# Kernel tuning notes

Hardware: AMD Instinct MI355X
Metric: run time of the kernel (lower is better)

Reference implementation:

```python
import jax, jax.numpy as jnp
import numpy as np

B, T, RES, C = 4, 8, 32, 128
TSP, SPLIT = 4, 4
NH_BRANCH = 4  # num_heads // 2 per branch
HID = 4 * C


def layer_norm(x, w, b, eps=1e-5):
    mu = x.mean(-1, keepdims=True)
    var = ((x - mu) ** 2).mean(-1, keepdims=True)
    return (x - mu) * jax.lax.rsqrt(var + eps) * w + b


def dwconv3d(x, w, b):
    # x: (Bw, C, Tsp, Hsp, Wsp); w: (C, 1, 3, 3, 3) depthwise
    y = jax.lax.conv_general_dilated(
        x, w, (1, 1, 1), 'SAME',
        dimension_numbers=('NCDHW', 'OIDHW', 'NCDHW'),
        feature_group_count=x.shape[1])
    return y + b[None, :, None, None, None]


def lepe_attention(q, k, v, conv_w, conv_b, Tsp, Hsp, Wsp, nh, Tt, H, W):
    Bq, L, Cc = q.shape
    hd = Cc // nh
    win = Tsp * Hsp * Wsp
    scale = float(hd) ** -0.5

    def to_win(z):
        z = z.reshape(Bq, Tt // Tsp, Tsp, H // Hsp, Hsp, W // Wsp, Wsp, Cc)
        z = z.transpose(0, 1, 3, 5, 2, 4, 6, 7).reshape(-1, win, nh, hd)
        return z.transpose(0, 2, 1, 3)

    qw = to_win(q) * scale
    kw = to_win(k)
    # v windows as (Bw, C, Tsp, Hsp, Wsp) for the depthwise-conv LePE
    vw5 = v.reshape(Bq, Tt // Tsp, Tsp, H // Hsp, Hsp, W // Wsp, Wsp, Cc)
    vw5 = vw5.transpose(0, 1, 3, 5, 7, 2, 4, 6).reshape(-1, Cc, Tsp, Hsp, Wsp)
    lepe = dwconv3d(vw5, conv_w, conv_b)

    def heads(z5):
        return z5.reshape(-1, nh, hd, win).transpose(0, 1, 3, 2)

    vh, lepeh = heads(vw5), heads(lepe)
    attn = jax.nn.softmax(jnp.einsum('bnqd,bnkd->bnqk', qw, kw), axis=-1)
    out = jnp.einsum('bnqk,bnkd->bnqd', attn, vh) + lepeh
    # windows -> video token order (T, H, W)
    out = out.transpose(0, 2, 1, 3).reshape(
        Bq, Tt // Tsp, H // Hsp, W // Wsp, Tsp, Hsp, Wsp, Cc)
    out = out.transpose(0, 1, 4, 2, 5, 3, 6, 7).reshape(Bq, L, Cc)
    return out


def setup_inputs() -> dict:
    key = jax.random.key(0)
    ks = jax.random.split(key, 16)
    L = T * RES * RES
    h = C // 2
    p = lambda k, s: jax.random.normal(k, s, dtype=jnp.float32) * 0.02
    return {
        'x': jax.random.normal(ks[0], (B, L, C), dtype=jnp.float32),
        'norm1_w': jnp.ones((C,), jnp.float32),
        'norm1_b': jnp.zeros((C,), jnp.float32),
        'qkv_w': p(ks[1], (3 * C, C)),
        'conv_w0': p(ks[2], (h, 1, 3, 3, 3)),
        'conv_b0': jnp.zeros((h,), jnp.float32),
        'conv_w1': p(ks[3], (h, 1, 3, 3, 3)),
        'conv_b1': jnp.zeros((h,), jnp.float32),
        'proj_w': p(ks[4], (C, C)),
        'proj_b': jnp.zeros((C,), jnp.float32),
        'norm2_w': jnp.ones((C,), jnp.float32),
        'norm2_b': jnp.zeros((C,), jnp.float32),
        'fc1_w': p(ks[5], (HID, C)),
        'fc1_b': jnp.zeros((HID,), jnp.float32),
        'fc2_w': p(ks[6], (C, HID)),
        'fc2_b': jnp.zeros((C,), jnp.float32),
    }


def reference(x, norm1_w, norm1_b, qkv_w, conv_w0, conv_b0, conv_w1, conv_b1,
              proj_w, proj_b, norm2_w, norm2_b, fc1_w, fc1_b, fc2_w, fc2_b):
    img = layer_norm(x, norm1_w, norm1_b)
    qkv = img @ qkv_w.T  # (B, L, 3C), split order q, k, v
    q, k, v = jnp.split(qkv, 3, axis=-1)
    h = C // 2
    # branch 0 (idx=0): H_sp = reso, W_sp = split_size
    x1 = lepe_attention(q[..., :h], k[..., :h], v[..., :h], conv_w0, conv_b0,
                        TSP, RES, SPLIT, NH_BRANCH, T, RES, RES)
    # branch 1 (idx=1): H_sp = split_size, W_sp = reso
    x2 = lepe_attention(q[..., h:], k[..., h:], v[..., h:], conv_w1, conv_b1,
                        TSP, SPLIT, RES, NH_BRANCH, T, RES, RES)
    att = jnp.concatenate([x1, x2], axis=2) @ proj_w.T + proj_b
    x = x + att
    y = layer_norm(x, norm2_w, norm2_b)
    y = jax.nn.gelu(y @ fc1_w.T + fc1_b, approximate=False) @ fc2_w.T + fc2_b
    return x + y
```

## Files before the change

kernel.cpp:

```cpp
#include <hip/hip_runtime.h>
#include <math.h>

namespace {
constexpr int C_ = 128;
constexpr int BL = 32768;

typedef __attribute__((ext_vector_type(4))) float f32x4;
typedef __attribute__((ext_vector_type(4))) _Float16 f16x4;
typedef __attribute__((ext_vector_type(8))) _Float16 f16x8;
typedef __attribute__((ext_vector_type(2))) __fp16 hf2;

#if __has_builtin(__builtin_amdgcn_exp2f)
#define EXP2F(x) __builtin_amdgcn_exp2f(x)
#else
#define EXP2F(x) exp2f(x)
#endif
}

__global__ __launch_bounds__(256) void k_cvt(
    const float* __restrict__ qkvw, const float* __restrict__ pw,
    const float* __restrict__ f1w,  const float* __restrict__ f2w,
    const float* __restrict__ cw0,  const float* __restrict__ cw1,
    _Float16* __restrict__ wqh, _Float16* __restrict__ pwh,
    _Float16* __restrict__ w1h, _Float16* __restrict__ w2h,
    float* __restrict__ lepw)
{
  int i = blockIdx.x * 256 + threadIdx.x;
  if (i < 49152) {
    float v = qkvw[i];
    if (i < 16384) v *= 0.360673762f;
    wqh[i] = (_Float16)v;
  }
  else if (i < 65536)  pwh[i - 49152] = (_Float16)pw[i - 49152];
  else if (i < 131072) w1h[i - 65536] = (_Float16)f1w[i - 65536];
  else if (i < 196608) w2h[i - 131072] = (_Float16)f2w[i - 131072];
  else if (i < 200064) {
    int j = i - 196608;
    int br = j / 1728, r = j % 1728, widx = r >> 6, ch = r & 63;
    lepw[j] = (br ? cw1 : cw0)[ch * 27 + widx];
  }
}

__global__ __launch_bounds__(256) void k_ln_qkv(
    const float* __restrict__ x,
    const float* __restrict__ nw,
    const float* __restrict__ nb,
    const _Float16* __restrict__ wqh,
    _Float16* __restrict__ qh, _Float16* __restrict__ kh, _Float16* __restrict__ vh)
{
  __shared__ _Float16 xs[64][136];
  __shared__ _Float16 qt[64][136];
  __shared__ _Float16 wbuf[128][136];
  const int tid = threadIdx.x;
  const int row0 = blockIdx.x << 6;
  const int bb = row0 >> 13, t = (row0 >> 10) & 7, h0 = (row0 >> 5) & 31;
  const int tb = t >> 2, t_in = t & 3;

  {
    const int r = tid >> 2, j = tid & 3;
    const float* xp = x + (size_t)(row0 + r) * C_ + j * 32;
    float v[32];
#pragma unroll
    for (int i = 0; i < 8; ++i) {
      float4 u = ((const float4*)xp)[i];
      v[i*4+0] = u.x; v[i*4+1] = u.y; v[i*4+2] = u.z; v[i*4+3] = u.w;
    }
    float s1 = 0.f, s2 = 0.f;
#pragma unroll
    for (int i = 0; i < 32; ++i) { s1 += v[i]; s2 += v[i] * v[i]; }
    s1 += __shfl_down(s1, 2, 4); s1 += __shfl_down(s1, 1, 4);
    s2 += __shfl_down(s2, 2, 4); s2 += __shfl_down(s2, 1, 4);
    float mu = __shfl(s1, 0, 4) * (1.f / 128.f);
    float ms = __shfl(s2, 0, 4) * (1.f / 128.f);
    float rstd = rsqrtf(ms - mu * mu + 1e-5f);
#pragma unroll
    for (int i = 0; i < 32; ++i) {
      int c = j * 32 + i;
      xs[r][c] = (_Float16)((v[i] - mu) * rstd * nw[c] + nb[c]);
    }
  }
  __syncthreads();

  const int lane = tid & 63, wave = tid >> 6;
  const int m0 = wave << 4, mi = lane & 15, quad = lane >> 4;

  f16x8 afr[4];
#pragma unroll
  for (int kt = 0; kt < 4; ++kt)
    afr[kt] = *(const f16x8*)&xs[m0 + mi][kt * 32 + quad * 8];

  for (int g = 0; g < 3; ++g) {
#pragma unroll
    for (int it = 0; it < 8; ++it) {
      int id = it * 256 + tid;
      int r = id >> 4, c8 = id & 15;
      *(uint4*)&wbuf[r][c8 * 8] = *(const uint4*)(wqh + (size_t)(g * 128 + r) * 128 + c8 * 8);
    }
    __syncthreads();

    f32x4 acc[8];
#pragma unroll
    for (int nt = 0; nt < 8; ++nt) acc[nt] = (f32x4){0.f, 0.f, 0.f, 0.f};
#pragma unroll
    for (int nt = 0; nt < 8; ++nt) {
#pragma unroll
      for (int kt = 0; kt < 4; ++kt) {
        f16x8 bfr = *(const f16x8*)&wbuf[nt * 16 + mi][kt * 32 + quad * 8];
        acc[nt] = __builtin_amdgcn_mfma_f32_16x16x32_f16(afr[kt], bfr, acc[nt], 0, 0, 0);
      }
    }
#pragma unroll
    for (int nt = 0; nt < 8; ++nt) {
      int n = nt * 16 + mi;
#pragma unroll
      for (int rr = 0; rr < 4; ++rr)
        qt[m0 + quad * 4 + rr][n] = (_Float16)acc[nt][rr];
    }
    __syncthreads();

    _Float16* G = (g == 0) ? qh : (g == 1) ? kh : vh;
#pragma unroll
    for (int it = 0; it < 4; ++it) {
      int u = it * 256 + tid;
      if (u < 512) {
        int half = u & 1, p = (u >> 1) & 7, head = (u >> 4) & 3, sb = u >> 6;
        int token = (p >> 2) * 32 + sb * 4 + (p & 3);
        uint4 d = *(const uint4*)&qt[token][head * 16 + half * 8];
        int win = bb * 16 + tb * 8 + sb;
        int pos = t_in * 128 + h0 * 4 + p;
        *(uint4*)(G + ((size_t)(head * 64 + win) * 512 + pos) * 16 + half * 8) = d;
      } else {
        int u2 = u - 512;
        int half = u2 & 1, pin = (u2 >> 1) & 63, head = u2 >> 7;
        uint4 d = *(const uint4*)&qt[pin][64 + head * 16 + half * 8];
        int win = bb * 16 + tb * 8 + (h0 >> 2);
        int pos = t_in * 128 + (h0 & 3) * 32 + pin;
        *(uint4*)(G + ((size_t)((4 + head) * 64 + win) * 512 + pos) * 16 + half * 8) = d;
      }
    }
    __syncthreads();
  }
}

__global__ __launch_bounds__(512) void k_attn(
    const _Float16* __restrict__ qh,
    const _Float16* __restrict__ kh,
    const _Float16* __restrict__ vh,
    const float* __restrict__ lepw,
    const float* __restrict__ cb0,
    const float* __restrict__ cb1,
    _Float16* __restrict__ attnh)
{
  __shared__ _Float16 Ks[512][20];
  __shared__ _Float16 Vs[512][20];

  const int tid = threadIdx.x;
  const int bid = blockIdx.x;
  const int br = bid >> 8, wi = (bid >> 2) & 63, head = bid & 3;
  const int b = wi >> 4, tb = (wi >> 3) & 1, sb = wi & 7;
  const int coff = br * 64 + head * 16;
  const int Hsp = br ? 4 : 32, Wsp = br ? 32 : 4;
  const float* cb = br ? cb1 : cb0;
  const size_t base = ((size_t)(br * 4 + head) * 64 + wi) * 512 * 16;

  auto token_of = [&](int p) -> int {
    int t_in = p >> 7;
    int rem = p & 127;
    int h, w;
    if (br == 0) { h = rem >> 2;            w = sb * 4 + (rem & 3); }
    else         { h = sb * 4 + (rem >> 5); w = rem & 31; }
    return ((b * 8 + tb * 4 + t_in) << 10) + (h << 5) + w;
  };

  {
    const int r = tid;
    const _Float16* kp = kh + base + r * 16;
    const _Float16* vp = vh + base + r * 16;
    f16x8 k0 = *(const f16x8*)kp;
    f16x8 k1 = *(const f16x8*)(kp + 8);
    f16x8 v0 = *(const f16x8*)vp;
    f16x8 v1 = *(const f16x8*)(vp + 8);
    *(f16x4*)&Ks[r][0]  = (f16x4){k0[0], k0[1], k0[2], k0[3]};
    *(f16x4*)&Ks[r][4]  = (f16x4){k0[4], k0[5], k0[6], k0[7]};
    *(f16x4*)&Ks[r][8]  = (f16x4){k1[0], k1[1], k1[2], k1[3]};
    *(f16x4*)&Ks[r][12] = (f16x4){k1[4], k1[5], k1[6], k1[7]};
    *(f16x4*)&Vs[r][0]  = (f16x4){v0[0], v0[1], v0[2], v0[3]};
    *(f16x4*)&Vs[r][4]  = (f16x4){v0[4], v0[5], v0[6], v0[7]};
    *(f16x4*)&Vs[r][8]  = (f16x4){v1[0], v1[1], v1[2], v1[3]};
    *(f16x4*)&Vs[r][12] = (f16x4){v1[4], v1[5], v1[6], v1[7]};
  }

  const int lane = tid & 63, wave = tid >> 6;
  const int mi = lane & 15, quad = lane >> 4;

  int qtok[4];
  f16x4 qfr[4];
#pragma unroll
  for (int qi = 0; qi < 4; ++qi) {
    int q = (wave * 4 + qi) * 16 + mi;
    qtok[qi] = token_of(q);
    qfr[qi] = *(const f16x4*)(qh + base + q * 16 + quad * 4);
  }
  __syncthreads();

  f32x4 acc[4];
  float l[4];
#pragma unroll
  for (int qi = 0; qi < 4; ++qi) { acc[qi] = (f32x4){0.f,0.f,0.f,0.f}; l[qi] = 0.f; }

  const hf2 one2 = {(__fp16)1.f, (__fp16)1.f};

  for (int kt = 0; kt < 32; ++kt) {
    const int kb = kt << 4;
    f16x4 kfr = *(const f16x4*)&Ks[kb + mi][quad * 4];
    f16x4 vfr;
    vfr[0] = Vs[kb + quad * 4 + 0][mi];
    vfr[1] = Vs[kb + quad * 4 + 1][mi];
    vfr[2] = Vs[kb + quad * 4 + 2][mi];
    vfr[3] = Vs[kb + quad * 4 + 3][mi];
#pragma unroll
    for (int qi = 0; qi < 4; ++qi) {
      f32x4 s = __builtin_amdgcn_mfma_f32_16x16x16f16(kfr, qfr[qi], (f32x4){0.f,0.f,0.f,0.f}, 0, 0, 0);
      float p0 = EXP2F(s[0]);
      float p1 = EXP2F(s[1]);
      float p2 = EXP2F(s[2]);
      float p3 = EXP2F(s[3]);
      hf2 plo = __builtin_amdgcn_cvt_pkrtz(p0, p1);
      hf2 phi = __builtin_amdgcn_cvt_pkrtz(p2, p3);
#if __has_builtin(__builtin_amdgcn_fdot2)
      l[qi] = __builtin_amdgcn_fdot2(plo, one2, l[qi], false);
      l[qi] = __builtin_amdgcn_fdot2(phi, one2, l[qi], false);
#else
      l[qi] += (p0 + p1) + (p2 + p3);
#endif
      union { struct { hf2 lo, hi; } h; f16x4 v; } u;
      u.h.lo = plo; u.h.hi = phi;
      acc[qi] = __builtin_amdgcn_mfma_f32_16x16x16f16(vfr, u.v, acc[qi], 0, 0, 0);
    }
  }

#pragma unroll
  for (int qi = 0; qi < 4; ++qi) {
    float lq = l[qi];
    lq += __shfl_xor(lq, 16, 64);
    lq += __shfl_xor(lq, 32, 64);
    float inv = 1.f / lq;

    const int q = (wave * 4 + qi) * 16 + mi;
    int t_in = q >> 7, rem = q & 127;
    int h_in, w_in;
    if (br == 0) { h_in = rem >> 2; w_in = rem & 3; }
    else         { h_in = rem >> 5; w_in = rem & 31; }
    float4 lep = *(const float4*)(cb + head * 16 + quad * 4);
    for (int dz = 0; dz < 3; ++dz) {
      int tz = t_in + dz - 1; if ((unsigned)tz >= 4u) continue;
      for (int dy = 0; dy < 3; ++dy) {
        int ty = h_in + dy - 1; if ((unsigned)ty >= (unsigned)Hsp) continue;
        for (int dx = 0; dx < 3; ++dx) {
          int tx = w_in + dx - 1; if ((unsigned)tx >= (unsigned)Wsp) continue;
          int np = (tz * Hsp + ty) * Wsp + tx;
          int widx = (dz * 3 + dy) * 3 + dx;
          float4 w4 = *(const float4*)(lepw + ((br * 27 + widx) << 6) + head * 16 + quad * 4);
          f16x4 vv = *(const f16x4*)&Vs[np][quad * 4];
          lep.x += w4.x * (float)vv[0];
          lep.y += w4.y * (float)vv[1];
          lep.z += w4.z * (float)vv[2];
          lep.w += w4.w * (float)vv[3];
        }
      }
    }
    f16x4 ov;
    ov[0] = (_Float16)(acc[qi][0] * inv + lep.x);
    ov[1] = (_Float16)(acc[qi][1] * inv + lep.y);
    ov[2] = (_Float16)(acc[qi][2] * inv + lep.z);
    ov[3] = (_Float16)(acc[qi][3] * inv + lep.w);
    *(f16x4*)(attnh + (size_t)qtok[qi] * 128 + coff + quad * 4) = ov;
  }
}

__global__ __launch_bounds__(256) void k_proj(
    const _Float16* __restrict__ attnh,
    const _Float16* __restrict__ pwh,
    const float* __restrict__ pb,
    const float* __restrict__ x,
    _Float16* __restrict__ xrh)
{
  __shared__ _Float16 as_[64][136];
  __shared__ _Float16 wbuf[128][136];
  const int tid = threadIdx.x;
  const int row0 = blockIdx.x << 6;

#pragma unroll
  for (int it = 0; it < 4; ++it) {
    int id = it * 256 + tid;
    int r = id >> 4, c8 = id & 15;
    *(uint4*)&as_[r][c8 * 8] = *(const uint4*)(attnh + (size_t)(row0 + r) * 128 + c8 * 8);
  }
#pragma unroll
  for (int it = 0; it < 8; ++it) {
    int id = it * 256 + tid;
    int r = id >> 4, c8 = id & 15;
    *(uint4*)&wbuf[r][c8 * 8] = *(const uint4*)(pwh + (size_t)r * 128 + c8 * 8);
  }
  __syncthreads();

  const int lane = tid & 63, wave = tid >> 6;
  const int m0 = wave << 4, mi = lane & 15, quad = lane >> 4;

  f16x8 afr[4];
#pragma unroll
  for (int kt = 0; kt < 4; ++kt)
    afr[kt] = *(const f16x8*)&as_[m0 + mi][kt * 32 + quad * 8];

  f32x4 acc[8];
#pragma unroll
  for (int nt = 0; nt < 8; ++nt) acc[nt] = (f32x4){0.f, 0.f, 0.f, 0.f};
#pragma unroll
  for (int nt = 0; nt < 8; ++nt) {
#pragma unroll
    for (int kt = 0; kt < 4; ++kt) {
      f16x8 bfr = *(const f16x8*)&wbuf[nt * 16 + mi][kt * 32 + quad * 8];
      acc[nt] = __builtin_amdgcn_mfma_f32_16x16x32_f16(afr[kt], bfr, acc[nt], 0, 0, 0);
    }
  }
  __syncthreads();
#pragma unroll
  for (int nt = 0; nt < 8; ++nt) {
    int n = nt * 16 + mi;
    float bb = pb[n];
#pragma unroll
    for (int rr = 0; rr < 4; ++rr)
      as_[m0 + quad * 4 + rr][n] = (_Float16)(acc[nt][rr] + bb);
  }
  __syncthreads();

#pragma unroll
  for (int it = 0; it < 4; ++it) {
    int id = it * 256 + tid;
    int r = id >> 4, c8 = id & 15;
    f16x8 v = *(const f16x8*)&as_[r][c8 * 8];
    const float* xp = x + (size_t)(row0 + r) * 128 + c8 * 8;
    float4 xa = *(const float4*)xp;
    float4 xb = *(const float4*)(xp + 4);
    f16x8 o;
    o[0] = (_Float16)((float)v[0] + xa.x); o[1] = (_Float16)((float)v[1] + xa.y);
    o[2] = (_Float16)((float)v[2] + xa.z); o[3] = (_Float16)((float)v[3] + xa.w);
    o[4] = (_Float16)((float)v[4] + xb.x); o[5] = (_Float16)((float)v[5] + xb.y);
    o[6] = (_Float16)((float)v[6] + xb.z); o[7] = (_Float16)((float)v[7] + xb.w);
    *(f16x8*)(xrh + (size_t)(row0 + r) * 128 + c8 * 8) = o;
  }
}

__global__ __launch_bounds__(256) void k_mlp(
    const _Float16* __restrict__ xrh,
    const float* __restrict__ nw,
    const float* __restrict__ nb,
    const _Float16* __restrict__ w1h,
    const float* __restrict__ f1b,
    const _Float16* __restrict__ w2h,
    const float* __restrict__ f2b,
    float* __restrict__ out)
{
  __shared__ _Float16 xs[64][136];
  __shared__ _Float16 wbuf[128][136];
  const int tid = threadIdx.x;
  const int row0 = blockIdx.x << 6;

  {
    const int r = tid >> 2, j = tid & 3;
    const _Float16* xp = xrh + (size_t)(row0 + r) * C_ + j * 32;
    float v[32];
#pragma unroll
    for (int i = 0; i < 4; ++i) {
      f16x8 u = ((const f16x8*)xp)[i];
#pragma unroll
      for (int k = 0; k < 8; ++k) v[i * 8 + k] = (float)u[k];
    }
    float s1 = 0.f, s2 = 0.f;
#pragma unroll
    for (int i = 0; i < 32; ++i) { s1 += v[i]; s2 += v[i] * v[i]; }
    s1 += __shfl_down(s1, 2, 4); s1 += __shfl_down(s1, 1, 4);
    s2 += __shfl_down(s2, 2, 4); s2 += __shfl_down(s2, 1, 4);
    float mu = __shfl(s1, 0, 4) * (1.f / 128.f);
    float ms = __shfl(s2, 0, 4) * (1.f / 128.f);
    float rstd = rsqrtf(ms - mu * mu + 1e-5f);
#pragma unroll
    for (int i = 0; i < 32; ++i) {
      int c = j * 32 + i;
      xs[r][c] = (_Float16)((v[i] - mu) * rstd * nw[c] + nb[c]);
    }
  }
  __syncthreads();

  const int lane = tid & 63, wave = tid >> 6;
  const int tok0 = wave << 4, mi = lane & 15, quad = lane >> 4;

  f16x8 bx[4];
#pragma unroll
  for (int kt = 0; kt < 4; ++kt)
    bx[kt] = *(const f16x8*)&xs[tok0 + mi][kt * 32 + quad * 8];

  f32x4 oacc[8];
#pragma unroll
  for (int o = 0; o < 8; ++o) oacc[o] = (f32x4){0.f, 0.f, 0.f, 0.f};

  for (int ng = 0; ng < 4; ++ng) {
#pragma unroll
    for (int it = 0; it < 8; ++it) {
      int id = it * 256 + tid;
      int r = id >> 4, c8 = id & 15;
      *(uint4*)&wbuf[r][c8 * 8] = *(const uint4*)(w1h + (size_t)(ng * 128 + r) * 128 + c8 * 8);
    }
    __syncthreads();

    f32x4 hacc[8];
#pragma unroll
    for (int t = 0; t < 8; ++t) hacc[t] = (f32x4){0.f, 0.f, 0.f, 0.f};
#pragma unroll
    for (int t = 0; t < 8; ++t) {
#pragma unroll
      for (int kt = 0; kt < 4; ++kt) {
        f16x8 wfr = *(const f16x8*)&wbuf[t * 16 + mi][kt * 32 + quad * 8];
        hacc[t] = __builtin_amdgcn_mfma_f32_16x16x32_f16(wfr, bx[kt], hacc[t], 0, 0, 0);
      }
    }
    f16x4 ph[8];
#pragma unroll
    for (int t = 0; t < 8; ++t) {
      float4 bj = *(const float4*)(f1b + ng * 128 + t * 16 + quad * 4);
      float h0v = hacc[t][0] + bj.x;
      float h1v = hacc[t][1] + bj.y;
      float h2v = hacc[t][2] + bj.z;
      float h3v = hacc[t][3] + bj.w;
      ph[t][0] = (_Float16)(0.5f * h0v * (1.f + erff(h0v * 0.70710678118654752f)));
      ph[t][1] = (_Float16)(0.5f * h1v * (1.f + erff(h1v * 0.70710678118654752f)));
      ph[t][2] = (_Float16)(0.5f * h2v * (1.f + erff(h2v * 0.70710678118654752f)));
      ph[t][3] = (_Float16)(0.5f * h3v * (1.f + erff(h3v * 0.70710678118654752f)));
    }
    __syncthreads();

#pragma unroll
    for (int it = 0; it < 8; ++it) {
      int id = it * 256 + tid;
      int r = id >> 4, c8 = id & 15;
      *(uint4*)&wbuf[r][c8 * 8] = *(const uint4*)(w2h + (size_t)r * 512 + ng * 128 + c8 * 8);
    }
    __syncthreads();

#pragma unroll
    for (int o = 0; o < 8; ++o) {
#pragma unroll
      for (int t = 0; t < 8; ++t) {
        f16x4 wfr = *(const f16x4*)&wbuf[o * 16 + mi][t * 16 + quad * 4];
        oacc[o] = __builtin_amdgcn_mfma_f32_16x16x16f16(wfr, ph[t], oacc[o], 0, 0, 0);
      }
    }
    __syncthreads();
  }

#pragma unroll
  for (int o = 0; o < 8; ++o) {
    int row = row0 + tok0 + mi;
    int cb4 = o * 16 + quad * 4;
    float4 bo = *(const float4*)(f2b + cb4);
    f16x4 res = *(const f16x4*)(xrh + (size_t)row * C_ + cb4);
    float4 ov;
    ov.x = oacc[o][0] + bo.x + (float)res[0];
    ov.y = oacc[o][1] + bo.y + (float)res[1];
    ov.z = oacc[o][2] + bo.z + (float)res[2];
    ov.w = oacc[o][3] + bo.w + (float)res[3];
    *(float4*)(out + (size_t)row * C_ + cb4) = ov;
  }
}

extern "C" void kernel_launch(void* const* d_in, const int* in_sizes, int n_in,
                              void* d_out, int out_size, void* d_ws, size_t ws_size,
                              hipStream_t stream)
{
  const float* x    = (const float*)d_in[0];
  const float* n1w  = (const float*)d_in[1];
  const float* n1b  = (const float*)d_in[2];
  const float* qkvw = (const float*)d_in[3];
  const float* cw0  = (const float*)d_in[4];
  const float* cb0  = (const float*)d_in[5];
  const float* cw1  = (const float*)d_in[6];
  const float* cb1  = (const float*)d_in[7];
  const float* pw   = (const float*)d_in[8];
  const float* pb   = (const float*)d_in[9];
  const float* n2w  = (const float*)d_in[10];
  const float* n2b  = (const float*)d_in[11];
  const float* f1w  = (const float*)d_in[12];
  const float* f1b  = (const float*)d_in[13];
  const float* f2w  = (const float*)d_in[14];
  const float* f2b  = (const float*)d_in[15];

  char* ws = (char*)d_ws;
  _Float16* qh    = (_Float16*)ws;
  _Float16* kh    = (_Float16*)(ws +  8388608);
  _Float16* vh    = (_Float16*)(ws + 16777216);
  _Float16* attnh = (_Float16*)(ws + 25165824);
  _Float16* xrh   = (_Float16*)(ws + 33554432);
  _Float16* wqh   = (_Float16*)(ws + 41943040);
  _Float16* pwh   = (_Float16*)(ws + 42041344);
  _Float16* w1h   = (_Float16*)(ws + 42074112);
  _Float16* w2h   = (_Float16*)(ws + 42205184);
  float*    lepw  = (float*)   (ws + 42336256);

  k_cvt   <<<782,     256, 0, stream>>>(qkvw, pw, f1w, f2w, cw0, cw1,
                                        wqh, pwh, w1h, w2h, lepw);
  k_ln_qkv<<<BL / 64, 256, 0, stream>>>(x, n1w, n1b, wqh, qh, kh, vh);
  k_attn  <<<512,     512, 0, stream>>>(qh, kh, vh, lepw, cb0, cb1, attnh);
  k_proj  <<<BL / 64, 256, 0, stream>>>(attnh, pwh, pb, x, xrh);
  k_mlp   <<<BL / 64, 256, 0, stream>>>(xrh, n2w, n2b, w1h, f1b, w2h, f2b,
                                        (float*)d_out);
}
```

Baseline: 197.1 us.

## Halve row tile to 32 tokens and split N across waves in GEMM kernels

The LN+QKV, projection and MLP kernels now process 32 rows per block instead of 64, with the four waves arranged as 2 M-tiles by 2 N-halves. This doubles the grid size to 1024 blocks so more blocks can be resident across the CUs, and it halves per-wave accumulator registers. The cost is that every weight tile in LDS is loaded twice as often per token, which adds global and LDS traffic. The head scatter in the QKV kernel is remapped for the smaller tile.

```diff
diff --git a/kernel.cpp b/kernel.cpp
--- a/kernel.cpp
+++ b/kernel.cpp
@@ -48,41 +48,42 @@
     const _Float16* __restrict__ wqh,
     _Float16* __restrict__ qh, _Float16* __restrict__ kh, _Float16* __restrict__ vh)
 {
-  __shared__ _Float16 xs[64][136];
-  __shared__ _Float16 qt[64][136];
+  __shared__ _Float16 xs[32][136];
+  __shared__ _Float16 qt[32][136];
   __shared__ _Float16 wbuf[128][136];
   const int tid = threadIdx.x;
-  const int row0 = blockIdx.x << 6;
+  const int row0 = blockIdx.x << 5;
   const int bb = row0 >> 13, t = (row0 >> 10) & 7, h0 = (row0 >> 5) & 31;
   const int tb = t >> 2, t_in = t & 3;
 
   {
-    const int r = tid >> 2, j = tid & 3;
-    const float* xp = x + (size_t)(row0 + r) * C_ + j * 32;
-    float v[32];
-#pragma unroll
-    for (int i = 0; i < 8; ++i) {
+    const int r = tid >> 3, j = tid & 7;
+    const float* xp = x + (size_t)(row0 + r) * C_ + j * 16;
+    float v[16];
+#pragma unroll
+    for (int i = 0; i < 4; ++i) {
       float4 u = ((const float4*)xp)[i];
       v[i*4+0] = u.x; v[i*4+1] = u.y; v[i*4+2] = u.z; v[i*4+3] = u.w;
     }
     float s1 = 0.f, s2 = 0.f;
 #pragma unroll
-    for (int i = 0; i < 32; ++i) { s1 += v[i]; s2 += v[i] * v[i]; }
-    s1 += __shfl_down(s1, 2, 4); s1 += __shfl_down(s1, 1, 4);
-    s2 += __shfl_down(s2, 2, 4); s2 += __shfl_down(s2, 1, 4);
-    float mu = __shfl(s1, 0, 4) * (1.f / 128.f);
-    float ms = __shfl(s2, 0, 4) * (1.f / 128.f);
+    for (int i = 0; i < 16; ++i) { s1 += v[i]; s2 += v[i] * v[i]; }
+    s1 += __shfl_down(s1, 4, 8); s1 += __shfl_down(s1, 2, 8); s1 += __shfl_down(s1, 1, 8);
+    s2 += __shfl_down(s2, 4, 8); s2 += __shfl_down(s2, 2, 8); s2 += __shfl_down(s2, 1, 8);
+    float mu = __shfl(s1, 0, 8) * (1.f / 128.f);
+    float ms = __shfl(s2, 0, 8) * (1.f / 128.f);
     float rstd = rsqrtf(ms - mu * mu + 1e-5f);
 #pragma unroll
-    for (int i = 0; i < 32; ++i) {
-      int c = j * 32 + i;
+    for (int i = 0; i < 16; ++i) {
+      int c = j * 16 + i;
       xs[r][c] = (_Float16)((v[i] - mu) * rstd * nw[c] + nb[c]);
     }
   }
   __syncthreads();
 
   const int lane = tid & 63, wave = tid >> 6;
-  const int m0 = wave << 4, mi = lane & 15, quad = lane >> 4;
+  const int mt = wave & 1, nh = wave >> 1;
+  const int m0 = mt << 4, mi = lane & 15, quad = lane >> 4;
 
   f16x8 afr[4];
 #pragma unroll
@@ -98,20 +99,21 @@
     }
     __syncthreads();
 
-    f32x4 acc[8];
-#pragma unroll
-    for (int nt = 0; nt < 8; ++nt) acc[nt] = (f32x4){0.f, 0.f, 0.f, 0.f};
-#pragma unroll
-    for (int nt = 0; nt < 8; ++nt) {
+    f32x4 acc[4];
+#pragma unroll
+    for (int nt = 0; nt < 4; ++nt) acc[nt] = (f32x4){0.f, 0.f, 0.f, 0.f};
+#pragma unroll
+    for (int nt = 0; nt < 4; ++nt) {
+      int wrow = (nh * 4 + nt) * 16 + mi;
 #pragma unroll
       for (int kt = 0; kt < 4; ++kt) {
-        f16x8 bfr = *(const f16x8*)&wbuf[nt * 16 + mi][kt * 32 + quad * 8];
+        f16x8 bfr = *(const f16x8*)&wbuf[wrow][kt * 32 + quad * 8];
         acc[nt] = __builtin_amdgcn_mfma_f32_16x16x32_f16(afr[kt], bfr, acc[nt], 0, 0, 0);
       }
     }
 #pragma unroll
-    for (int nt = 0; nt < 8; ++nt) {
-      int n = nt * 16 + mi;
+    for (int nt = 0; nt < 4; ++nt) {
+      int n = (nh * 4 + nt) * 16 + mi;
 #pragma unroll
       for (int rr = 0; rr < 4; ++rr)
         qt[m0 + quad * 4 + rr][n] = (_Float16)acc[nt][rr];
@@ -120,21 +122,20 @@
 
     _Float16* G = (g == 0) ? qh : (g == 1) ? kh : vh;
 #pragma unroll
-    for (int it = 0; it < 4; ++it) {
+    for (int it = 0; it < 2; ++it) {
       int u = it * 256 + tid;
-      if (u < 512) {
-        int half = u & 1, p = (u >> 1) & 7, head = (u >> 4) & 3, sb = u >> 6;
-        int token = (p >> 2) * 32 + sb * 4 + (p & 3);
-        uint4 d = *(const uint4*)&qt[token][head * 16 + half * 8];
-        int win = bb * 16 + tb * 8 + sb;
-        int pos = t_in * 128 + h0 * 4 + p;
+      if (u < 256) {
+        int half = u & 1, w = (u >> 1) & 31, head = u >> 6;
+        uint4 d = *(const uint4*)&qt[w][head * 16 + half * 8];
+        int win = bb * 16 + tb * 8 + (w >> 2);
+        int pos = t_in * 128 + h0 * 4 + (w & 3);
         *(uint4*)(G + ((size_t)(head * 64 + win) * 512 + pos) * 16 + half * 8) = d;
       } else {
-        int u2 = u - 512;
-        int half = u2 & 1, pin = (u2 >> 1) & 63, head = u2 >> 7;
-        uint4 d = *(const uint4*)&qt[pin][64 + head * 16 + half * 8];
+        int u2 = u - 256;
+        int half = u2 & 1, w = (u2 >> 1) & 31, head = u2 >> 6;
+        uint4 d = *(const uint4*)&qt[w][64 + head * 16 + half * 8];
         int win = bb * 16 + tb * 8 + (h0 >> 2);
-        int pos = t_in * 128 + (h0 & 3) * 32 + pin;
+        int pos = t_in * 128 + (h0 & 3) * 32 + w;
         *(uint4*)(G + ((size_t)((4 + head) * 64 + win) * 512 + pos) * 16 + half * 8) = d;
       }
     }
@@ -285,13 +286,13 @@
     const float* __restrict__ x,
     _Float16* __restrict__ xrh)
 {
-  __shared__ _Float16 as_[64][136];
+  __shared__ _Float16 as_[32][136];
   __shared__ _Float16 wbuf[128][136];
   const int tid = threadIdx.x;
-  const int row0 = blockIdx.x << 6;
-
-#pragma unroll
-  for (int it = 0; it < 4; ++it) {
+  const int row0 = blockIdx.x << 5;
+
+#pragma unroll
+  for (int it = 0; it < 2; ++it) {
     int id = it * 256 + tid;
     int r = id >> 4, c8 = id & 15;
     *(uint4*)&as_[r][c8 * 8] = *(const uint4*)(attnh + (size_t)(row0 + r) * 128 + c8 * 8);
@@ -305,28 +306,30 @@
   __syncthreads();
 
   const int lane = tid & 63, wave = tid >> 6;
-  const int m0 = wave << 4, mi = lane & 15, quad = lane >> 4;
+  const int mt = wave & 1, nh = wave >> 1;
+  const int m0 = mt << 4, mi = lane & 15, quad = lane >> 4;
 
   f16x8 afr[4];
 #pragma unroll
   for (int kt = 0; kt < 4; ++kt)
     afr[kt] = *(const f16x8*)&as_[m0 + mi][kt * 32 + quad * 8];
 
-  f32x4 acc[8];
-#pragma unroll
-  for (int nt = 0; nt < 8; ++nt) acc[nt] = (f32x4){0.f, 0.f, 0.f, 0.f};
-#pragma unroll
-  for (int nt = 0; nt < 8; ++nt) {
+  f32x4 acc[4];
+#pragma unroll
+  for (int nt = 0; nt < 4; ++nt) acc[nt] = (f32x4){0.f, 0.f, 0.f, 0.f};
+#pragma unroll
+  for (int nt = 0; nt < 4; ++nt) {
+    int wrow = (nh * 4 + nt) * 16 + mi;
 #pragma unroll
     for (int kt = 0; kt < 4; ++kt) {
-      f16x8 bfr = *(const f16x8*)&wbuf[nt * 16 + mi][kt * 32 + quad * 8];
+      f16x8 bfr = *(const f16x8*)&wbuf[wrow][kt * 32 + quad * 8];
       acc[nt] = __builtin_amdgcn_mfma_f32_16x16x32_f16(afr[kt], bfr, acc[nt], 0, 0, 0);
     }
   }
   __syncthreads();
 #pragma unroll
-  for (int nt = 0; nt < 8; ++nt) {
-    int n = nt * 16 + mi;
+  for (int nt = 0; nt < 4; ++nt) {
+    int n = (nh * 4 + nt) * 16 + mi;
     float bb = pb[n];
 #pragma unroll
     for (int rr = 0; rr < 4; ++rr)
@@ -335,7 +338,7 @@
   __syncthreads();
 
 #pragma unroll
-  for (int it = 0; it < 4; ++it) {
+  for (int it = 0; it < 2; ++it) {
     int id = it * 256 + tid;
     int r = id >> 4, c8 = id & 15;
     f16x8 v = *(const f16x8*)&as_[r][c8 * 8];
@@ -361,48 +364,49 @@
     const float* __restrict__ f2b,
     float* __restrict__ out)
 {
-  __shared__ _Float16 xs[64][136];
+  __shared__ _Float16 xs[32][136];
   __shared__ _Float16 wbuf[128][136];
   const int tid = threadIdx.x;
-  const int row0 = blockIdx.x << 6;
+  const int row0 = blockIdx.x << 5;
 
   {
-    const int r = tid >> 2, j = tid & 3;
-    const _Float16* xp = xrh + (size_t)(row0 + r) * C_ + j * 32;
-    float v[32];
-#pragma unroll
-    for (int i = 0; i < 4; ++i) {
+    const int r = tid >> 3, j = tid & 7;
+    const _Float16* xp = xrh + (size_t)(row0 + r) * C_ + j * 16;
+    float v[16];
+#pragma unroll
+    for (int i = 0; i < 2; ++i) {
       f16x8 u = ((const f16x8*)xp)[i];
 #pragma unroll
       for (int k = 0; k < 8; ++k) v[i * 8 + k] = (float)u[k];
     }
     float s1 = 0.f, s2 = 0.f;
 #pragma unroll
-    for (int i = 0; i < 32; ++i) { s1 += v[i]; s2 += v[i] * v[i]; }
-    s1 += __shfl_down(s1, 2, 4); s1 += __shfl_down(s1, 1, 4);
-    s2 += __shfl_down(s2, 2, 4); s2 += __shfl_down(s2, 1, 4);
-    float mu = __shfl(s1, 0, 4) * (1.f / 128.f);
-    float ms = __shfl(s2, 0, 4) * (1.f / 128.f);
+    for (int i = 0; i < 16; ++i) { s1 += v[i]; s2 += v[i] * v[i]; }
+    s1 += __shfl_down(s1, 4, 8); s1 += __shfl_down(s1, 2, 8); s1 += __shfl_down(s1, 1, 8);
+    s2 += __shfl_down(s2, 4, 8); s2 += __shfl_down(s2, 2, 8); s2 += __shfl_down(s2, 1, 8);
+    float mu = __shfl(s1, 0, 8) * (1.f / 128.f);
+    float ms = __shfl(s2, 0, 8) * (1.f / 128.f);
     float rstd = rsqrtf(ms - mu * mu + 1e-5f);
 #pragma unroll
-    for (int i = 0; i < 32; ++i) {
-      int c = j * 32 + i;
+    for (int i = 0; i < 16; ++i) {
+      int c = j * 16 + i;
       xs[r][c] = (_Float16)((v[i] - mu) * rstd * nw[c] + nb[c]);
     }
   }
   __syncthreads();
 
   const int lane = tid & 63, wave = tid >> 6;
-  const int tok0 = wave << 4, mi = lane & 15, quad = lane >> 4;
+  const int mt = wave & 1, oh = wave >> 1;
+  const int tok0 = mt << 4, mi = lane & 15, quad = lane >> 4;
 
   f16x8 bx[4];
 #pragma unroll
   for (int kt = 0; kt < 4; ++kt)
     bx[kt] = *(const f16x8*)&xs[tok0 + mi][kt * 32 + quad * 8];
 
-  f32x4 oacc[8];
-#pragma unroll
-  for (int o = 0; o < 8; ++o) oacc[o] = (f32x4){0.f, 0.f, 0.f, 0.f};
+  f32x4 oacc[4];
+#pragma unroll
+  for (int o = 0; o < 4; ++o) oacc[o] = (f32x4){0.f, 0.f, 0.f, 0.f};
 
   for (int ng = 0; ng < 4; ++ng) {
 #pragma unroll
@@ -448,10 +452,11 @@
     __syncthreads();
 
 #pragma unroll
-    for (int o = 0; o < 8; ++o) {
+    for (int o = 0; o < 4; ++o) {
+      int wrow = (oh * 4 + o) * 16 + mi;
 #pragma unroll
       for (int t = 0; t < 8; ++t) {
-        f16x4 wfr = *(const f16x4*)&wbuf[o * 16 + mi][t * 16 + quad * 4];
+        f16x4 wfr = *(const f16x4*)&wbuf[wrow][t * 16 + quad * 4];
         oacc[o] = __builtin_amdgcn_mfma_f32_16x16x16f16(wfr, ph[t], oacc[o], 0, 0, 0);
       }
     }
@@ -459,9 +464,9 @@
   }
 
 #pragma unroll
-  for (int o = 0; o < 8; ++o) {
+  for (int o = 0; o < 4; ++o) {
     int row = row0 + tok0 + mi;
-    int cb4 = o * 16 + quad * 4;
+    int cb4 = (oh * 4 + o) * 16 + quad * 4;
     float4 bo = *(const float4*)(f2b + cb4);
     f16x4 res = *(const f16x4*)(xrh + (size_t)row * C_ + cb4);
     float4 ov;
@@ -508,9 +513,9 @@
 
   k_cvt   <<<782,     256, 0, stream>>>(qkvw, pw, f1w, f2w, cw0, cw1,
                                         wqh, pwh, w1h, w2h, lepw);
-  k_ln_qkv<<<BL / 64, 256, 0, stream>>>(x, n1w, n1b, wqh, qh, kh, vh);
+  k_ln_qkv<<<BL / 32, 256, 0, stream>>>(x, n1w, n1b, wqh, qh, kh, vh);
   k_attn  <<<512,     512, 0, stream>>>(qh, kh, vh, lepw, cb0, cb1, attnh);
-  k_proj  <<<BL / 64, 256, 0, stream>>>(attnh, pwh, pb, x, xrh);
-  k_mlp   <<<BL / 64, 256, 0, stream>>>(xrh, n2w, n2b, w1h, f1b, w2h, f2b,
+  k_proj  <<<BL / 32, 256, 0, stream>>>(attnh, pwh, pb, x, xrh);
+  k_mlp   <<<BL / 32, 256, 0, stream>>>(xrh, n2w, n2b, w1h, f1b, w2h, f2b,
                                         (float*)d_out);
 }
```

Result: no change. 199.9 us (+1.4%).

## Split MLP hidden dimension across two wave groups with shared-memory reduction

Applied to the files above, without the earlier changes.

The MLP kernel moves from 256 to 512 threads per block. The two halves of the waves each handle half of every 128-wide hidden chunk for the same 16 tokens, and the partial fc2 accumulators are reduced through shared memory before the epilogue. The aim is more waves per block and fewer accumulator and hidden registers per wave, which should improve latency hiding. The cost is an extra shared-memory reduction pass and a sync, and the reduction buffer (32 KB) must fit in wbuf, which it does.

```diff
diff --git a/kernel.cpp b/kernel.cpp
--- a/kernel.cpp
+++ b/kernel.cpp
@@ -351,7 +351,7 @@
   }
 }
 
-__global__ __launch_bounds__(256) void k_mlp(
+__global__ __launch_bounds__(512) void k_mlp(
     const _Float16* __restrict__ xrh,
     const float* __restrict__ nw,
     const float* __restrict__ nb,
@@ -367,33 +367,34 @@
   const int row0 = blockIdx.x << 6;
 
   {
-    const int r = tid >> 2, j = tid & 3;
-    const _Float16* xp = xrh + (size_t)(row0 + r) * C_ + j * 32;
-    float v[32];
-#pragma unroll
-    for (int i = 0; i < 4; ++i) {
+    const int r = tid >> 3, j = tid & 7;
+    const _Float16* xp = xrh + (size_t)(row0 + r) * C_ + j * 16;
+    float v[16];
+#pragma unroll
+    for (int i = 0; i < 2; ++i) {
       f16x8 u = ((const f16x8*)xp)[i];
 #pragma unroll
       for (int k = 0; k < 8; ++k) v[i * 8 + k] = (float)u[k];
     }
     float s1 = 0.f, s2 = 0.f;
 #pragma unroll
-    for (int i = 0; i < 32; ++i) { s1 += v[i]; s2 += v[i] * v[i]; }
-    s1 += __shfl_down(s1, 2, 4); s1 += __shfl_down(s1, 1, 4);
-    s2 += __shfl_down(s2, 2, 4); s2 += __shfl_down(s2, 1, 4);
-    float mu = __shfl(s1, 0, 4) * (1.f / 128.f);
-    float ms = __shfl(s2, 0, 4) * (1.f / 128.f);
+    for (int i = 0; i < 16; ++i) { s1 += v[i]; s2 += v[i] * v[i]; }
+    s1 += __shfl_down(s1, 4, 8); s1 += __shfl_down(s1, 2, 8); s1 += __shfl_down(s1, 1, 8);
+    s2 += __shfl_down(s2, 4, 8); s2 += __shfl_down(s2, 2, 8); s2 += __shfl_down(s2, 1, 8);
+    float mu = __shfl(s1, 0, 8) * (1.f / 128.f);
+    float ms = __shfl(s2, 0, 8) * (1.f / 128.f);
     float rstd = rsqrtf(ms - mu * mu + 1e-5f);
 #pragma unroll
-    for (int i = 0; i < 32; ++i) {
-      int c = j * 32 + i;
+    for (int i = 0; i < 16; ++i) {
+      int c = j * 16 + i;
       xs[r][c] = (_Float16)((v[i] - mu) * rstd * nw[c] + nb[c]);
     }
   }
   __syncthreads();
 
   const int lane = tid & 63, wave = tid >> 6;
-  const int tok0 = wave << 4, mi = lane & 15, quad = lane >> 4;
+  const int mt = wave & 3, hh = wave >> 2;
+  const int tok0 = mt << 4, mi = lane & 15, quad = lane >> 4;
 
   f16x8 bx[4];
 #pragma unroll
@@ -406,28 +407,29 @@
 
   for (int ng = 0; ng < 4; ++ng) {
 #pragma unroll
-    for (int it = 0; it < 8; ++it) {
-      int id = it * 256 + tid;
+    for (int it = 0; it < 4; ++it) {
+      int id = it * 512 + tid;
       int r = id >> 4, c8 = id & 15;
       *(uint4*)&wbuf[r][c8 * 8] = *(const uint4*)(w1h + (size_t)(ng * 128 + r) * 128 + c8 * 8);
     }
     __syncthreads();
 
-    f32x4 hacc[8];
-#pragma unroll
-    for (int t = 0; t < 8; ++t) hacc[t] = (f32x4){0.f, 0.f, 0.f, 0.f};
-#pragma unroll
-    for (int t = 0; t < 8; ++t) {
+    f32x4 hacc[4];
+#pragma unroll
+    for (int t = 0; t < 4; ++t) hacc[t] = (f32x4){0.f, 0.f, 0.f, 0.f};
+#pragma unroll
+    for (int t = 0; t < 4; ++t) {
+      int hrow = hh * 64 + t * 16 + mi;
 #pragma unroll
       for (int kt = 0; kt < 4; ++kt) {
-        f16x8 wfr = *(const f16x8*)&wbuf[t * 16 + mi][kt * 32 + quad * 8];
+        f16x8 wfr = *(const f16x8*)&wbuf[hrow][kt * 32 + quad * 8];
         hacc[t] = __builtin_amdgcn_mfma_f32_16x16x32_f16(wfr, bx[kt], hacc[t], 0, 0, 0);
       }
     }
-    f16x4 ph[8];
-#pragma unroll
-    for (int t = 0; t < 8; ++t) {
-      float4 bj = *(const float4*)(f1b + ng * 128 + t * 16 + quad * 4);
+    f16x4 ph[4];
+#pragma unroll
+    for (int t = 0; t < 4; ++t) {
+      float4 bj = *(const float4*)(f1b + ng * 128 + hh * 64 + t * 16 + quad * 4);
       float h0v = hacc[t][0] + bj.x;
       float h1v = hacc[t][1] + bj.y;
       float h2v = hacc[t][2] + bj.z;
@@ -440,8 +442,8 @@
     __syncthreads();
 
 #pragma unroll
-    for (int it = 0; it < 8; ++it) {
-      int id = it * 256 + tid;
+    for (int it = 0; it < 4; ++it) {
+      int id = it * 512 + tid;
       int r = id >> 4, c8 = id & 15;
       *(uint4*)&wbuf[r][c8 * 8] = *(const uint4*)(w2h + (size_t)r * 512 + ng * 128 + c8 * 8);
     }
@@ -450,26 +452,43 @@
 #pragma unroll
     for (int o = 0; o < 8; ++o) {
 #pragma unroll
-      for (int t = 0; t < 8; ++t) {
-        f16x4 wfr = *(const f16x4*)&wbuf[o * 16 + mi][t * 16 + quad * 4];
+      for (int t = 0; t < 4; ++t) {
+        f16x4 wfr = *(const f16x4*)&wbuf[o * 16 + mi][(hh * 4 + t) * 16 + quad * 4];
         oacc[o] = __builtin_amdgcn_mfma_f32_16x16x16f16(wfr, ph[t], oacc[o], 0, 0, 0);
       }
     }
     __syncthreads();
   }
 
-#pragma unroll
-  for (int o = 0; o < 8; ++o) {
-    int row = row0 + tok0 + mi;
-    int cb4 = o * 16 + quad * 4;
-    float4 bo = *(const float4*)(f2b + cb4);
-    f16x4 res = *(const f16x4*)(xrh + (size_t)row * C_ + cb4);
-    float4 ov;
-    ov.x = oacc[o][0] + bo.x + (float)res[0];
-    ov.y = oacc[o][1] + bo.y + (float)res[1];
-    ov.z = oacc[o][2] + bo.z + (float)res[2];
-    ov.w = oacc[o][3] + bo.w + (float)res[3];
-    *(float4*)(out + (size_t)row * C_ + cb4) = ov;
+  float* rbuf = (float*)wbuf;
+  if (hh == 1) {
+#pragma unroll
+    for (int o = 0; o < 8; ++o)
+#pragma unroll
+      for (int k = 0; k < 4; ++k)
+        rbuf[(o * 4 + k) * 256 + mt * 64 + lane] = oacc[o][k];
+  }
+  __syncthreads();
+  if (hh == 0) {
+#pragma unroll
+    for (int o = 0; o < 8; ++o)
+#pragma unroll
+      for (int k = 0; k < 4; ++k)
+        oacc[o][k] += rbuf[(o * 4 + k) * 256 + mt * 64 + lane];
+
+#pragma unroll
+    for (int o = 0; o < 8; ++o) {
+      int row = row0 + tok0 + mi;
+      int cb4 = o * 16 + quad * 4;
+      float4 bo = *(const float4*)(f2b + cb4);
+      f16x4 res = *(const f16x4*)(xrh + (size_t)row * C_ + cb4);
+      float4 ov;
+      ov.x = oacc[o][0] + bo.x + (float)res[0];
+      ov.y = oacc[o][1] + bo.y + (float)res[1];
+      ov.z = oacc[o][2] + bo.z + (float)res[2];
+      ov.w = oacc[o][3] + bo.w + (float)res[3];
+      *(float4*)(out + (size_t)row * C_ + cb4) = ov;
+    }
   }
 }
 
@@ -511,6 +530,6 @@
   k_ln_qkv<<<BL / 64, 256, 0, stream>>>(x, n1w, n1b, wqh, qh, kh, vh);
   k_attn  <<<512,     512, 0, stream>>>(qh, kh, vh, lepw, cb0, cb1, attnh);
   k_proj  <<<BL / 64, 256, 0, stream>>>(attnh, pwh, pb, x, xrh);
-  k_mlp   <<<BL / 64, 256, 0, stream>>>(xrh, n2w, n2b, w1h, f1b, w2h, f2b,
+  k_mlp   <<<BL / 64, 512, 0, stream>>>(xrh, n2w, n2b, w1h, f1b, w2h, f2b,
                                         (float*)d_out);
 }
```

After: 194.4 us. No clear change (-1.4%).
